# Performance work log

Hardware: AMD Instinct MI355X
Metric: run time of the kernel (lower is better)

Reference implementation:

```python
import jax, jax.numpy as jnp
import numpy as np

DIM = 1024
H = 16
D = DIM // H
SCALE = D ** -0.5
EPS = 1e-5


def _layernorm(x, w, b):
    # force_fp32 LayerNorm over last axis
    xf = x.astype(jnp.float32)
    mu = xf.mean(-1, keepdims=True)
    var = xf.var(-1, keepdims=True)
    y = (xf - mu) / jnp.sqrt(var + EPS) * w.astype(jnp.float32) + b.astype(jnp.float32)
    return y.astype(x.dtype)


def setup_inputs() -> dict:
    key = jax.random.key(0)
    ks = jax.random.split(key, 8)
    x = jax.random.normal(ks[0], (2, 2048, DIM), dtype=jnp.float32)
    qkv_w = jax.random.normal(ks[1], (3 * DIM, DIM), dtype=jnp.float32) * (DIM ** -0.5)
    q_norm_w = jnp.ones((D,), jnp.float32)
    q_norm_b = jnp.zeros((D,), jnp.float32)
    k_norm_w = jnp.ones((D,), jnp.float32)
    k_norm_b = jnp.zeros((D,), jnp.float32)
    proj_w = jax.random.normal(ks[2], (DIM, DIM), dtype=jnp.float32) * (DIM ** -0.5)
    proj_b = jnp.zeros((DIM,), jnp.float32)
    return {"x": x, "qkv_w": qkv_w, "q_norm_w": q_norm_w, "q_norm_b": q_norm_b,
            "k_norm_w": k_norm_w, "k_norm_b": k_norm_b, "proj_w": proj_w, "proj_b": proj_b}


def reference(x, qkv_w, q_norm_w, q_norm_b, k_norm_w, k_norm_b, proj_w, proj_b):
    B, N, C = x.shape
    qkv = x @ qkv_w.T                                  # [B,N,3C]
    qkv = qkv.reshape(B, N, 3, H, D).transpose(2, 0, 3, 1, 4)  # [3,B,H,N,D]
    q, k, v = qkv[0], qkv[1], qkv[2]
    # per-head QK LayerNorm over head_dim
    q = _layernorm(q, q_norm_w, q_norm_b)
    k = _layernorm(k, k_norm_w, k_norm_b)
    # k-centering across sequence
    k = k - k.mean(-2, keepdims=True)
    attn = jnp.einsum('bhnd,bhmd->bhnm', q * SCALE, k)
    attn = attn - attn.max(-1, keepdims=True)
    attn = jax.nn.softmax(attn, axis=-1)
    out = jnp.einsum('bhnm,bhmd->bhnd', attn, v)       # [B,H,N,D]
    out = out.transpose(0, 2, 1, 3).reshape(B, N, C)
    return out @ proj_w.T + proj_b
```

## Files before the change

### kernel.cpp

```cpp
#include <hip/hip_runtime.h>
#include <cstdint>
#include <cstddef>

#define SEQ     2048
#define NBATCH  2
#define CDIM    1024
#define NHEAD   16
#define HDIM    64
#define MTOT    (NBATCH*SEQ)
#define C3      (3*CDIM)
#define LOG2E   1.44269504088896340736f
#define QKSCALE (0.125f*LOG2E)
#define LN_EPS  1e-5f

typedef unsigned short u16;
typedef short s16x8 __attribute__((ext_vector_type(8)));
typedef float f32x4  __attribute__((ext_vector_type(4)));
typedef float f32x16 __attribute__((ext_vector_type(16)));

static __device__ __forceinline__ f32x4 mfma16(s16x8 a, s16x8 b, f32x4 c) {
  return __builtin_amdgcn_mfma_f32_16x16x32_bf16(a, b, c, 0, 0, 0);
}
static __device__ __forceinline__ f32x16 mfma32(s16x8 a, s16x8 b, f32x16 c) {
  return __builtin_amdgcn_mfma_f32_32x32x16_bf16(a, b, c, 0, 0, 0);
}
static __device__ __forceinline__ float b2f(u16 v) {
  return __uint_as_float(((unsigned)v) << 16);
}
static __device__ __forceinline__ u16 f2b(float f) {
  unsigned u = __float_as_uint(f);
  u = u + 0x7fffu + ((u >> 16) & 1u);
  return (u16)(u >> 16);
}
static __device__ __forceinline__ float fexp2(float x) {
  float r;
  asm("v_exp_f32 %0, %1" : "=v"(r) : "v"(x));
  return r;
}

#define G2L16(g, l) __builtin_amdgcn_global_load_lds( \
    (__attribute__((address_space(1))) void*)(g),     \
    (__attribute__((address_space(3))) void*)(l), 16, 0, 0)

#define XSEG   (MTOT*CDIM/8)
#define W1SEG  (C3*CDIM/8)
#define W2SEG  (CDIM*CDIM/8)
__global__ __launch_bounds__(256) void cast_all(
    const float* __restrict__ x, const float* __restrict__ w1,
    const float* __restrict__ w2, u16* __restrict__ xb,
    u16* __restrict__ wqkv, u16* __restrict__ wproj)
{
  int i = blockIdx.x * 256 + threadIdx.x;
  const float* src; u16* dst; int off;
  if (i < XSEG)              { src = x;  dst = xb;    off = i; }
  else if (i < XSEG + W1SEG) { src = w1; dst = wqkv;  off = i - XSEG; }
  else                       { src = w2; dst = wproj; off = i - XSEG - W1SEG; }
  float4 a = ((const float4*)src)[2*off];
  float4 b = ((const float4*)src)[2*off+1];
  union { u16 u[8]; uint4 v; } r;
  r.u[0]=f2b(a.x); r.u[1]=f2b(a.y); r.u[2]=f2b(a.z); r.u[3]=f2b(a.w);
  r.u[4]=f2b(b.x); r.u[5]=f2b(b.y); r.u[6]=f2b(b.z); r.u[7]=f2b(b.w);
  ((uint4*)dst)[off] = r.v;
}

template<bool WRITE_BF16, bool BIAS>
__global__ __launch_bounds__(256) void gemm_nt(
    const u16* __restrict__ A, const u16* __restrict__ Bm,
    void* __restrict__ Cout, const float* __restrict__ bias,
    int M, int Nn, int K)
{
  __shared__ u16 As[128*64];
  __shared__ u16 Bs[128*64];
  const int tid = threadIdx.x;
  const int wave = tid >> 6, lane = tid & 63;
  const int l15 = lane & 15, l4 = lane >> 4;
  const int m0 = blockIdx.x * 128, n0 = blockIdx.y * 128;
  const int wr = (wave >> 1) * 64, wc = (wave & 1) * 64;
  f32x4 acc[4][4] = {};

  for (int k0 = 0; k0 < K; k0 += 64) {
    if (k0) __syncthreads();
#pragma unroll
    for (int i = 0; i < 4; ++i) {
      int ci  = (i*4 + wave)*64 + lane;
      int row = ci >> 3, ch = ci & 7;
      int chs = ch ^ (row & 7);
      const u16* ga = A  + (size_t)(m0 + row)*K + k0 + chs*8;
      const u16* gb = Bm + (size_t)(n0 + row)*K + k0 + chs*8;
      G2L16(ga, As + (i*4 + wave)*512);
      G2L16(gb, Bs + (i*4 + wave)*512);
    }
    __syncthreads();

#pragma unroll
    for (int kk = 0; kk < 2; ++kk) {
      s16x8 af[4], bf[4];
#pragma unroll
      for (int r = 0; r < 4; ++r) {
        int row = wr + r*16 + l15;
        af[r] = *(const s16x8*)(As + row*64 + (((kk*4 + l4) ^ (row & 7))*8));
      }
#pragma unroll
      for (int c = 0; c < 4; ++c) {
        int row = wc + c*16 + l15;
        bf[c] = *(const s16x8*)(Bs + row*64 + (((kk*4 + l4) ^ (row & 7))*8));
      }
#pragma unroll
      for (int r = 0; r < 4; ++r)
#pragma unroll
        for (int c = 0; c < 4; ++c)
          acc[r][c] = mfma16(af[r], bf[c], acc[r][c]);
    }
  }

#pragma unroll
  for (int r = 0; r < 4; ++r)
#pragma unroll
    for (int c = 0; c < 4; ++c) {
      int row = m0 + wr + r*16 + l4*4;
      int col = n0 + wc + c*16 + l15;
#pragma unroll
      for (int q = 0; q < 4; ++q) {
        float v = acc[r][c][q];
        if (BIAS) v += bias[col];
        if (WRITE_BF16) ((u16*)Cout)[(size_t)(row + q)*Nn + col] = f2b(v);
        else           ((float*)Cout)[(size_t)(row + q)*Nn + col] = v;
      }
    }
}

__global__ __launch_bounds__(256) void ln_qk(
    const u16* __restrict__ qkv,
    const float* __restrict__ qw, const float* __restrict__ qb,
    const float* __restrict__ kw, const float* __restrict__ kb,
    u16* __restrict__ Qs, u16* __restrict__ Kn)
{
  int gw   = blockIdx.x * 4 + (threadIdx.x >> 6);
  int lane = threadIdx.x & 63;
  int m = gw >> 4, h = gw & 15;
  const u16* rowp = qkv + (size_t)m*C3 + h*HDIM + lane;
  int b = m >> 11, n = m & 2047;
  size_t o = ((size_t)(b*NHEAD + h)*SEQ + n)*HDIM + lane;

  float wq = qw[lane], bq = qb[lane], wk = kw[lane], bk = kb[lane];
  float xq = b2f(rowp[0]);
  float xk = b2f(rowp[CDIM]);
  float sq = xq, s2q = xq*xq, sk = xk, s2k = xk*xk;
#pragma unroll
  for (int off = 32; off; off >>= 1) {
    sq += __shfl_xor(sq, off, 64);  s2q += __shfl_xor(s2q, off, 64);
    sk += __shfl_xor(sk, off, 64);  s2k += __shfl_xor(s2k, off, 64);
  }
  float muq = sq*(1.f/64.f), varq = s2q*(1.f/64.f) - muq*muq;
  float muk = sk*(1.f/64.f), vark = s2k*(1.f/64.f) - muk*muk;
  float yq = (xq - muq) * (1.f/sqrtf(varq + LN_EPS)) * wq + bq;
  float yk = (xk - muk) * (1.f/sqrtf(vark + LN_EPS)) * wk + bk;
  Qs[o] = f2b(yq * QKSCALE);
  Kn[o] = f2b(yk);
}

__global__ __launch_bounds__(256) void v_transpose(
    const u16* __restrict__ qkv, u16* __restrict__ Vt)
{
  __shared__ u16 t[64][80];
  int bh = blockIdx.x, j0 = blockIdx.y * 64;
  int b = bh >> 4, h = bh & 15;
  int tid = threadIdx.x;
  int nl = tid >> 2, ch = tid & 3;
  const u16* src = qkv + (size_t)(b*SEQ + j0 + nl)*C3 + 2*CDIM + h*HDIM + ch*16;
  *(uint4*)&t[nl][ch*16]     = *(const uint4*)src;
  *(uint4*)&t[nl][ch*16 + 8] = *(const uint4*)(src + 8);
  __syncthreads();
  int d = tid >> 2, nc = tid & 3;
  u16 o[16];
#pragma unroll
  for (int i = 0; i < 16; ++i) o[i] = t[nc*16 + i][d];
  u16* dst = Vt + ((size_t)(bh*HDIM + d))*SEQ + j0 + nc*16;
  *(uint4*)dst       = *(uint4*)&o[0];
  *(uint4*)(dst + 8) = *(uint4*)&o[8];
}

__global__ __launch_bounds__(128) void flash_attn(
    const u16* __restrict__ Qs, const u16* __restrict__ Kn,
    const u16* __restrict__ Vt, u16* __restrict__ Oa)
{
  __shared__ u16 Kt[2][64*64];
  __shared__ u16 Vs[2][64*64];
  const int tid = threadIdx.x, wave = tid >> 6, lane = tid & 63;
  const int l31 = lane & 31, hi = lane >> 5;
  const int bh = blockIdx.y, q0 = blockIdx.x*64 + wave*32;
  const int sw = l31 & 7;

  const u16* Qrow = Qs + ((size_t)bh*SEQ + q0 + l31)*HDIM + hi*8;
  s16x8 qf[4];
#pragma unroll
  for (int ks = 0; ks < 4; ++ks)
    qf[ks] = *(const s16x8*)(Qrow + ks*16);

  f32x16 o0 = {}, o1 = {};
  float l_run = 0.f;

  const u16* Kg = Kn + (size_t)bh*SEQ*HDIM;
  const u16* Vg = Vt + (size_t)bh*HDIM*SEQ;

  auto STAGE = [&](int jb, int buf) {
#pragma unroll
    for (int i = 0; i < 4; ++i) {
      int ci = (i*2 + wave)*64 + lane;
      int row = ci >> 3, ch = ci & 7;
      int chs = ch ^ (row & 7);
      G2L16(Kg + (size_t)(jb + row)*HDIM + chs*8, Kt[buf] + (i*2 + wave)*512);
      G2L16(Vg + (size_t)row*SEQ + jb + chs*8,    Vs[buf] + (i*2 + wave)*512);
    }
  };

  STAGE(0, 0);
  __syncthreads();

  const int NT = SEQ/64;
  for (int t = 0; t < NT; ++t) {
    const int buf = t & 1;
    if (t + 1 < NT) STAGE((t+1)*64, buf ^ 1);
    const u16* Kb = Kt[buf];
    const u16* Vb = Vs[buf];

    f32x16 s0 = {}, s1 = {};
    __builtin_amdgcn_s_setprio(1);
#pragma unroll
    for (int ks = 0; ks < 4; ++ks) {
      int ch = ((ks*2 + hi) ^ sw) * 8;
      s16x8 k0 = *(const s16x8*)(Kb + l31*64 + ch);
      s16x8 k1 = *(const s16x8*)(Kb + (32 + l31)*64 + ch);
      s0 = mfma32(k0, qf[ks], s0);
      s1 = mfma32(k1, qf[ks], s1);
    }
    __builtin_amdgcn_s_setprio(0);

    float p0[16], p1[16];
#pragma unroll
    for (int i = 0; i < 16; ++i) p0[i] = fexp2(s0[i]);
#pragma unroll
    for (int i = 0; i < 16; ++i) p1[i] = fexp2(s1[i]);
    float s8[8];
#pragma unroll
    for (int i = 0; i < 8; ++i) s8[i] = (p0[i] + p0[i+8]) + (p1[i] + p1[i+8]);
    l_run += ((s8[0]+s8[1]) + (s8[2]+s8[3])) + ((s8[4]+s8[5]) + (s8[6]+s8[7]));

    s16x8 pf[4];
#pragma unroll
    for (int f = 0; f < 2; ++f) {
      const float* pp = f ? p1 : p0;
      unsigned pk[4][2];
#pragma unroll
      for (int q = 0; q < 4; ++q)
#pragma unroll
        for (int i = 0; i < 2; ++i)
          asm("v_cvt_pk_bf16_f32 %0, %1, %2"
              : "=v"(pk[q][i]) : "v"(pp[4*q+2*i]), "v"(pp[4*q+2*i+1]));
#pragma unroll
      for (int kc = 0; kc < 2; ++kc) {
        union { unsigned u[4]; s16x8 v; } bfu;
#pragma unroll
        for (int i = 0; i < 2; ++i) {
          unsigned x = pk[2*kc][i], y = pk[2*kc+1][i];
          asm("v_permlane32_swap_b32 %0, %1" : "+v"(x), "+v"(y));
          bfu.u[i] = x; bfu.u[2+i] = y;
        }
        pf[2*f+kc] = bfu.v;
      }
    }

    __builtin_amdgcn_s_setprio(1);
#pragma unroll
    for (int s = 0; s < 4; ++s) {
      int ch = ((s*2 + hi) ^ sw) * 8;
      s16x8 v0 = *(const s16x8*)(Vb + l31*64 + ch);
      s16x8 v1 = *(const s16x8*)(Vb + (32 + l31)*64 + ch);
      o0 = mfma32(v0, pf[s], o0);
      o1 = mfma32(v1, pf[s], o1);
    }
    __builtin_amdgcn_s_setprio(0);
    __syncthreads();
  }

  float l_all = l_run + __shfl_xor(l_run, 32, 64);
  float inv = 1.f / l_all;
  int b = bh >> 4, h = bh & 15;
  u16* dst = Oa + ((size_t)(b*SEQ + q0 + l31))*CDIM + h*HDIM;
#pragma unroll
  for (int df = 0; df < 2; ++df)
#pragma unroll
    for (int q2 = 0; q2 < 4; ++q2) {
      float a0, a1, a2, a3;
      if (df) { a0=o1[4*q2]; a1=o1[4*q2+1]; a2=o1[4*q2+2]; a3=o1[4*q2+3]; }
      else    { a0=o0[4*q2]; a1=o0[4*q2+1]; a2=o0[4*q2+2]; a3=o0[4*q2+3]; }
      a0 *= inv; a1 *= inv; a2 *= inv; a3 *= inv;
      unsigned w0, w1;
      asm("v_cvt_pk_bf16_f32 %0, %1, %2" : "=v"(w0) : "v"(a0), "v"(a1));
      asm("v_cvt_pk_bf16_f32 %0, %1, %2" : "=v"(w1) : "v"(a2), "v"(a3));
      uint2 st; st.x = w0; st.y = w1;
      *(uint2*)(dst + df*32 + q2*8 + hi*4) = st;
    }
}

extern "C" void kernel_launch(void* const* d_in, const int* in_sizes, int n_in,
                              void* d_out, int out_size, void* d_ws, size_t ws_size,
                              hipStream_t stream)
{
  const float* x      = (const float*)d_in[0];
  const float* qkv_w  = (const float*)d_in[1];
  const float* qnw    = (const float*)d_in[2];
  const float* qnb    = (const float*)d_in[3];
  const float* knw    = (const float*)d_in[4];
  const float* knb    = (const float*)d_in[5];
  const float* proj_w = (const float*)d_in[6];
  const float* proj_b = (const float*)d_in[7];
  float* out = (float*)d_out;

  char* ws = (char*)d_ws;
  u16* xb    = (u16*)(ws);
  u16* wqkv  = (u16*)(ws + (8ull  << 20));
  u16* wproj = (u16*)(ws + (14ull << 20));
  u16* qkvb  = (u16*)(ws + (16ull << 20));
  u16* Qsb   = (u16*)(ws + (40ull << 20));
  u16* Knb   = (u16*)(ws + (48ull << 20));
  u16* Vtb   = (u16*)(ws + (56ull << 20));
  u16* Oab   = (u16*)(ws + (64ull << 20));

  cast_all<<<(XSEG + W1SEG + W2SEG)/256, 256, 0, stream>>>(
      x, qkv_w, proj_w, xb, wqkv, wproj);

  gemm_nt<true, false><<<dim3(MTOT/128, C3/128), 256, 0, stream>>>(
      xb, wqkv, qkvb, nullptr, MTOT, C3, CDIM);

  ln_qk<<<(MTOT*NHEAD)/4, 256, 0, stream>>>(qkvb, qnw, qnb, knw, knb, Qsb, Knb);
  v_transpose<<<dim3(NBATCH*NHEAD, SEQ/64), 256, 0, stream>>>(qkvb, Vtb);

  flash_attn<<<dim3(SEQ/64, NBATCH*NHEAD), 128, 0, stream>>>(Qsb, Knb, Vtb, Oab);

  gemm_nt<false, true><<<dim3(MTOT/128, CDIM/128), 256, 0, stream>>>(
      Oab, wproj, out, proj_b, MTOT, CDIM, CDIM);
}
```

Measured before the change: 217.4 us.

## Vectorize QK layernorm and enlarge flash-attention blocks with XCD-aware block remap

```diff
diff --git a/kernel.cpp b/kernel.cpp
--- a/kernel.cpp
+++ b/kernel.cpp
@@ -135,28 +135,40 @@
     const float* __restrict__ kw, const float* __restrict__ kb,
     u16* __restrict__ Qs, u16* __restrict__ Kn)
 {
-  int gw   = blockIdx.x * 4 + (threadIdx.x >> 6);
-  int lane = threadIdx.x & 63;
-  int m = gw >> 4, h = gw & 15;
-  const u16* rowp = qkv + (size_t)m*C3 + h*HDIM + lane;
-  int b = m >> 11, n = m & 2047;
-  size_t o = ((size_t)(b*NHEAD + h)*SEQ + n)*HDIM + lane;
-
-  float wq = qw[lane], bq = qb[lane], wk = kw[lane], bk = kb[lane];
-  float xq = b2f(rowp[0]);
-  float xk = b2f(rowp[CDIM]);
-  float sq = xq, s2q = xq*xq, sk = xk, s2k = xk*xk;
-#pragma unroll
-  for (int off = 32; off; off >>= 1) {
-    sq += __shfl_xor(sq, off, 64);  s2q += __shfl_xor(s2q, off, 64);
-    sk += __shfl_xor(sk, off, 64);  s2k += __shfl_xor(s2k, off, 64);
+  const int tid = threadIdx.x, wave = tid >> 6, lane = tid & 63;
+  const int m = blockIdx.x*2 + (wave >> 1);
+  const int part = wave & 1;
+  const int b = m >> 11, n = m & 2047;
+  const float* wv = part ? kw : qw;
+  const float* bv = part ? kb : qb;
+  u16* dst = part ? Kn : Qs;
+  const float scale = part ? 1.f : QKSCALE;
+  const u16* base = qkv + (size_t)m*C3 + part*CDIM;
+  const int d0 = (lane & 7) * 8;
+  float wl[8], bl[8];
+#pragma unroll
+  for (int j = 0; j < 8; ++j) { wl[j] = wv[d0+j]*scale; bl[j] = bv[d0+j]*scale; }
+#pragma unroll
+  for (int c = 0; c < 2; ++c) {
+    int h = c*8 + (lane >> 3);
+    s16x8 v = *(const s16x8*)(base + c*512 + lane*8);
+    float f[8]; float s = 0.f, s2 = 0.f;
+#pragma unroll
+    for (int j = 0; j < 8; ++j) {
+      f[j] = b2f((u16)v[j]); s += f[j]; s2 += f[j]*f[j];
+    }
+#pragma unroll
+    for (int off = 1; off < 8; off <<= 1) {
+      s += __shfl_xor(s, off, 64); s2 += __shfl_xor(s2, off, 64);
+    }
+    float mu = s*(1.f/64.f);
+    float rs = rsqrtf(s2*(1.f/64.f) - mu*mu + LN_EPS);
+    union { u16 u[8]; uint4 q; } r;
+#pragma unroll
+    for (int j = 0; j < 8; ++j)
+      r.u[j] = f2b((f[j]-mu)*rs*wl[j] + bl[j]);
+    *(uint4*)(dst + ((size_t)(b*NHEAD+h)*SEQ + n)*HDIM + d0) = r.q;
   }
-  float muq = sq*(1.f/64.f), varq = s2q*(1.f/64.f) - muq*muq;
-  float muk = sk*(1.f/64.f), vark = s2k*(1.f/64.f) - muk*muk;
-  float yq = (xq - muq) * (1.f/sqrtf(varq + LN_EPS)) * wq + bq;
-  float yk = (xk - muk) * (1.f/sqrtf(vark + LN_EPS)) * wk + bk;
-  Qs[o] = f2b(yq * QKSCALE);
-  Kn[o] = f2b(yk);
 }
 
 __global__ __launch_bounds__(256) void v_transpose(
@@ -180,7 +192,7 @@
   *(uint4*)(dst + 8) = *(uint4*)&o[8];
 }
 
-__global__ __launch_bounds__(128) void flash_attn(
+__global__ __launch_bounds__(256) void flash_attn(
     const u16* __restrict__ Qs, const u16* __restrict__ Kn,
     const u16* __restrict__ Vt, u16* __restrict__ Oa)
 {
@@ -188,7 +200,10 @@
   __shared__ u16 Vs[2][64*64];
   const int tid = threadIdx.x, wave = tid >> 6, lane = tid & 63;
   const int l31 = lane & 31, hi = lane >> 5;
-  const int bh = blockIdx.y, q0 = blockIdx.x*64 + wave*32;
+  const int bid0 = blockIdx.x + blockIdx.y*16;
+  const int nid  = (bid0 & 7)*64 + (bid0 >> 3);
+  const int bh   = nid >> 4;
+  const int q0   = (nid & 15)*128 + wave*32;
   const int sw = l31 & 7;
 
   const u16* Qrow = Qs + ((size_t)bh*SEQ + q0 + l31)*HDIM + hi*8;
@@ -205,12 +220,12 @@
 
   auto STAGE = [&](int jb, int buf) {
 #pragma unroll
-    for (int i = 0; i < 4; ++i) {
-      int ci = (i*2 + wave)*64 + lane;
+    for (int i = 0; i < 2; ++i) {
+      int ci = (i*4 + wave)*64 + lane;
       int row = ci >> 3, ch = ci & 7;
       int chs = ch ^ (row & 7);
-      G2L16(Kg + (size_t)(jb + row)*HDIM + chs*8, Kt[buf] + (i*2 + wave)*512);
-      G2L16(Vg + (size_t)row*SEQ + jb + chs*8,    Vs[buf] + (i*2 + wave)*512);
+      G2L16(Kg + (size_t)(jb + row)*HDIM + chs*8, Kt[buf] + (i*4 + wave)*512);
+      G2L16(Vg + (size_t)row*SEQ + jb + chs*8,    Vs[buf] + (i*4 + wave)*512);
     }
   };
 
@@ -333,10 +348,10 @@
   gemm_nt<true, false><<<dim3(MTOT/128, C3/128), 256, 0, stream>>>(
       xb, wqkv, qkvb, nullptr, MTOT, C3, CDIM);
 
-  ln_qk<<<(MTOT*NHEAD)/4, 256, 0, stream>>>(qkvb, qnw, qnb, knw, knb, Qsb, Knb);
+  ln_qk<<<MTOT/2, 256, 0, stream>>>(qkvb, qnw, qnb, knw, knb, Qsb, Knb);
   v_transpose<<<dim3(NBATCH*NHEAD, SEQ/64), 256, 0, stream>>>(qkvb, Vtb);
 
-  flash_attn<<<dim3(SEQ/64, NBATCH*NHEAD), 128, 0, stream>>>(Qsb, Knb, Vtb, Oab);
+  flash_attn<<<dim3(SEQ/128, NBATCH*NHEAD), 256, 0, stream>>>(Qsb, Knb, Vtb, Oab);
 
   gemm_nt<false, true><<<dim3(MTOT/128, CDIM/128), 256, 0, stream>>>(
       Oab, wproj, out, proj_b, MTOT, CDIM, CDIM);
```

New measurement: 198.5 us. 1.1x faster.
